# Performance work log

Measured on AMD Instinct MI355X. Metric: run time of the kernel, lower is better.

Reference implementation:

```python
import jax, jax.numpy as jnp
import numpy as np

MUL = 512
IR_DIMS = (1, 3, 5)          # 0e, 1e, 2e -> 2l+1
PW = MUL ** -0.5             # path_weight = (mul_in * n_paths_to_out)^-0.5, n_paths=1 each


def setup_inputs() -> dict:
    key = jax.random.key(0)
    k_x, k0, k1, k2 = jax.random.split(key, 4)
    B = 4096
    D = MUL * sum(IR_DIMS)  # 4608
    return {
        "x": jax.random.normal(k_x, (B, D), dtype=jnp.float32),
        "w0": jax.random.normal(k0, (MUL, MUL), dtype=jnp.float32),
        "w1": jax.random.normal(k1, (MUL, MUL), dtype=jnp.float32),
        "w2": jax.random.normal(k2, (MUL, MUL), dtype=jnp.float32),
        "b0": jnp.zeros((MUL,), dtype=jnp.float32),  # bias only on scalar 0e irrep
    }


def reference(x, w0, w1, w2, b0):
    B = x.shape[0]
    # split x into per-irrep blocks (B, mul, 2l+1), as Irreps.as_list does
    offs = np.cumsum([0] + [MUL * d for d in IR_DIMS])
    blocks = [x[:, offs[i]:offs[i + 1]].reshape(B, MUL, IR_DIMS[i]) for i in range(3)]
    outs = []
    for blk, w, d in zip(blocks, (w0, w1, w2), IR_DIMS):
        # path_weight * einsum('uw,bui->bwi'), then flatten to mul_ir_out.dim
        o = PW * jnp.einsum('uw,bui->bwi', w, blk)
        outs.append(o.reshape(B, MUL * d))
    # bias instruction: path_weight 1.0, only on the scalar (0e) output irrep
    outs[0] = outs[0] + b0[None, :]
    return jnp.concatenate(outs, axis=-1)
```

## Files before the change

### kernel.cpp

```cpp
#include <hip/hip_runtime.h>


#define BATCH 4096
#define DTOT 4608
#define NMUL 512

typedef __attribute__((ext_vector_type(8))) short short8;
typedef __attribute__((ext_vector_type(8))) unsigned short ushort8;
typedef __attribute__((ext_vector_type(4))) float float4v;

#define XPL_BYTES (9ull * BATCH * NMUL * 2)

__device__ __forceinline__ unsigned short f2bf(float f) {
    unsigned int u = __builtin_bit_cast(unsigned int, f);
    return (unsigned short)((u + 0x7fffu + ((u >> 16) & 1u)) >> 16);
}
__device__ __forceinline__ void gld16(const unsigned short* g, unsigned short* l) {
    __builtin_amdgcn_global_load_lds(
        (const __attribute__((address_space(1))) unsigned int*)(const void*)g,
        (__attribute__((address_space(3))) unsigned int*)(void*)l, 16, 0, 0);
}
__device__ __forceinline__ void waitvm0() {
    asm volatile("s_waitcnt vmcnt(0)" ::: "memory");
}
__device__ __forceinline__ void waitlgkm0() {
    asm volatile("s_waitcnt lgkmcnt(0)" ::: "memory");
}
__device__ __forceinline__ void colmap(int col, int& c, int& u) {
    if (col < 512)       { c = 0; u = col; }
    else if (col < 2048) { int t = col - 512;  c = 1 + t % 3; u = t / 3; }
    else                 { int t = col - 2048; c = 4 + t % 5; u = t / 5; }
}

__global__ __launch_bounds__(256) void prep(const float* __restrict__ x,
                                            const float* __restrict__ w0,
                                            const float* __restrict__ w1,
                                            const float* __restrict__ w2,
                                            unsigned short* __restrict__ Xp,
                                            unsigned short* __restrict__ Wt) {
    __shared__ unsigned short buf[4608];
    const int tid = threadIdx.x;
    const int b = blockIdx.x;
    if (b < BATCH) {
        const int row = b;
        const float4v* src = (const float4v*)(x + (size_t)row * DTOT);
        for (int p = tid; p < DTOT / 4; p += 256) {
            float4v v = src[p];
#pragma unroll
            for (int j = 0; j < 4; ++j) {
                int c, u; colmap(p * 4 + j, c, u);
                buf[c * NMUL + u] = f2bf(v[j]);
            }
        }
        __syncthreads();
        for (int q = tid; q < DTOT / 8; q += 256) {
            const int c = q >> 6, u8 = q & 63;
            *(ushort8*)(Xp + ((size_t)(c * BATCH + row) * NMUL) + u8 * 8) =
                *(const ushort8*)&buf[c * NMUL + u8 * 8];
        }
    } else {
        const int t = b - BATCH;
        const int ch = t >> 6, tt = t & 63;
        const int tk = (tt >> 3) * 64, tn = (tt & 7) * 64;
        const float* W = (ch == 0) ? w0 : (ch == 1) ? w1 : w2;
        const int r0 = tid >> 4, c4 = (tid & 15) * 4;
#pragma unroll
        for (int rr = 0; rr < 4; ++rr) {
            const int row = r0 + rr * 16;
            float4v v = *(const float4v*)(W + (size_t)(tk + row) * NMUL + tn + c4);
#pragma unroll
            for (int j = 0; j < 4; ++j) buf[(c4 + j) * 72 + row] = f2bf(v[j]);
        }
        __syncthreads();
        for (int q = tid; q < 512; q += 256) {
            const int nn = q >> 3, k8 = q & 7;
            *(ushort8*)(Wt + ((size_t)(ch * NMUL + tn + nn) * NMUL) + tk + k8 * 8) =
                *(const ushort8*)&buf[nn * 72 + k8 * 8];
        }
    }
}

template <int MI>
__device__ __forceinline__ void kloop(const unsigned short* __restrict__ Ag,
                                      const unsigned short* __restrict__ Bg,
                                      unsigned short* Aw, unsigned short* Bw,
                                      int lr, int lq, int rsw,
                                      float4v (*acc)[4]) {
    for (int kt = 0; kt < 16; ++kt) {
        const int ko = kt * 32;
#pragma unroll
        for (int p = 0; p < MI; ++p)
            gld16(Ag + (size_t)p * 16 * NMUL + ko, Aw + p * 512);
#pragma unroll
        for (int p = 0; p < 4; ++p)
            gld16(Bg + (size_t)p * 16 * NMUL + ko, Bw + p * 512);
        waitvm0();
        short8 af[MI], bf[4];
#pragma unroll
        for (int mi = 0; mi < MI; ++mi)
            af[mi] = *(const short8*)(Aw + (mi * 16 + lr) * 32 + rsw);
#pragma unroll
        for (int ni = 0; ni < 4; ++ni)
            bf[ni] = *(const short8*)(Bw + (ni * 16 + lr) * 32 + rsw);
        __builtin_amdgcn_s_setprio(1);
#pragma unroll
        for (int mi = 0; mi < MI; ++mi)
#pragma unroll
            for (int ni = 0; ni < 4; ++ni)
                acc[mi][ni] = __builtin_amdgcn_mfma_f32_16x16x32_bf16(
                    af[mi], bf[ni], acc[mi][ni], 0, 0, 0);
        __builtin_amdgcn_s_setprio(0);
        waitlgkm0();
    }
}

template <int D, int XOFF>
__device__ __forceinline__ void epi(int tid, int w, int lr, int lq,
                                    int m0, int n0,
                                    float4v (*acc)[4], float* Cs,
                                    float* __restrict__ out) {
    const float PW = 0.044194173824159216f;
    __syncthreads();
#pragma unroll
    for (int mc = 0; mc < 4; ++mc) {
        if (w < D) {
#pragma unroll
            for (int ni = 0; ni < 4; ++ni)
#pragma unroll
                for (int r = 0; r < 4; ++r)
                    Cs[(lq * 4 + r) * (64 * D) + (ni * 16 + lr) * D + w] =
                        acc[mc][ni][r] * PW;
        }
        __syncthreads();
        constexpr int F4 = 16 * 16 * D;
        for (int f = tid; f < F4; f += 320) {
            const int row = f / (16 * D);
            const int c4  = f % (16 * D);
            *(float4v*)(out + (size_t)(m0 + mc * 16 + row) * DTOT + XOFF + n0 * D + c4 * 4) =
                *(const float4v*)(Cs + f * 4);
        }
        __syncthreads();
    }
}

__global__ __launch_bounds__(320) void gemm_all(const unsigned short* __restrict__ Xp,
                                                const unsigned short* __restrict__ Wt,
                                                const float* __restrict__ b0,
                                                float* __restrict__ out) {
    __shared__ __align__(16) unsigned short As[20480];

    const int hw = blockIdx.x;
    const int xcd = hw & 7, j = hw >> 3;
    const int b = ((xcd + ((j >> 3) << 3)) << 3) + (j & 7);

    const int tid = threadIdx.x;
    const int lane = tid & 63;
    const int w = tid >> 6;
    const int lr = lane & 15;
    const int lq = lane >> 4;
    const int ksw = ((lane & 3) ^ ((lane >> 3) & 3)) * 8;
    const int rsw = (lq ^ ((lr >> 1) & 3)) * 8;

    unsigned short* Aw = As + w * 4096;
    unsigned short* Bw = Aw + 2048;

    const bool isD5 = (b < 512);
    const int rel = isD5 ? b : b - 512;
    const int m0 = (rel >> 3) * 64;
    const int n0 = (rel & 7) * 64;

    float4v acc[4][4];
#pragma unroll
    for (int a = 0; a < 4; ++a)
#pragma unroll
        for (int c = 0; c < 4; ++c) acc[a][c] = (float4v)0.f;

    if (isD5) {
        const unsigned short* Ag =
            Xp + ((size_t)(4 + w) * BATCH + m0 + (lane >> 2)) * NMUL + ksw;
        const unsigned short* Bg =
            Wt + ((size_t)2 * NMUL + n0 + (lane >> 2)) * NMUL + ksw;
        kloop<4>(Ag, Bg, Aw, Bw, lr, lq, rsw, acc);
        epi<5, 2048>(tid, w, lr, lq, m0, n0, acc, (float*)As, out);
    } else {
        if (w < 3) {
            const unsigned short* Ag =
                Xp + ((size_t)(1 + w) * BATCH + m0 + (lane >> 2)) * NMUL + ksw;
            const unsigned short* Bg =
                Wt + ((size_t)1 * NMUL + n0 + (lane >> 2)) * NMUL + ksw;
            kloop<4>(Ag, Bg, Aw, Bw, lr, lq, rsw, acc);
        } else {
            const int mb = m0 + (w - 3) * 32;
            const unsigned short* Ag =
                Xp + ((size_t)0 * BATCH + mb + (lane >> 2)) * NMUL + ksw;
            const unsigned short* Bg =
                Wt + ((size_t)0 * NMUL + n0 + (lane >> 2)) * NMUL + ksw;
            kloop<2>(Ag, Bg, Aw, Bw, lr, lq, rsw, acc);
            const float PW = 0.044194173824159216f;
#pragma unroll
            for (int ni = 0; ni < 4; ++ni) {
                const int col = n0 + ni * 16 + lr;
                const float bias = b0[col];
#pragma unroll
                for (int mi = 0; mi < 2; ++mi)
#pragma unroll
                    for (int r = 0; r < 4; ++r)
                        out[(size_t)(mb + mi * 16 + lq * 4 + r) * DTOT + col] =
                            acc[mi][ni][r] * PW + bias;
            }
        }
        epi<3, 512>(tid, w, lr, lq, m0, n0, acc, (float*)As, out);
    }
}

extern "C" void kernel_launch(void* const* d_in, const int* in_sizes, int n_in,
                              void* d_out, int out_size, void* d_ws, size_t ws_size,
                              hipStream_t stream) {
    const float* x  = (const float*)d_in[0];
    const float* w0 = (const float*)d_in[1];
    const float* w1 = (const float*)d_in[2];
    const float* w2 = (const float*)d_in[3];
    const float* b0 = (const float*)d_in[4];
    float* out = (float*)d_out;

    unsigned short* Xp = (unsigned short*)d_ws;
    unsigned short* Wt = (unsigned short*)((char*)d_ws + XPL_BYTES);

    prep<<<dim3(BATCH + 192), dim3(256), 0, stream>>>(x, w0, w1, w2, Xp, Wt);
    gemm_all<<<dim3(1024), dim3(320), 0, stream>>>(Xp, Wt, b0, out);
}
```

Before: 182.3 us.

## Reorganize GEMM into large shared-B tiles with double-buffered LDS pipeline

The packed X layout is changed so each irrep's components sit interleaved per batch row, which turns each irrep block into one tall GEMM with M = B·(2l+1). The GEMM kernel now uses 512-thread blocks with large tiles (BM×256) that share the B tile across eight waves, replacing per-wave private tiles. Loads are staged with K-step 64 and double-buffered, using partial vmcnt waits so the next tile's loads overlap the current tile's MFMAs. The aim is more operand reuse and less per-wave load latency, at the cost of higher LDS use (128KB), fewer blocks (416) and a more complex epilogue that de-interleaves components through LDS.

```diff
diff --git a/kernel.cpp b/kernel.cpp
--- a/kernel.cpp
+++ b/kernel.cpp
@@ -20,8 +20,9 @@
         (const __attribute__((address_space(1))) unsigned int*)(const void*)g,
         (__attribute__((address_space(3))) unsigned int*)(void*)l, 16, 0, 0);
 }
-__device__ __forceinline__ void waitvm0() {
-    asm volatile("s_waitcnt vmcnt(0)" ::: "memory");
+template <int N>
+__device__ __forceinline__ void waitvm() {
+    asm volatile("s_waitcnt vmcnt(%0)" :: "n"(N) : "memory");
 }
 __device__ __forceinline__ void waitlgkm0() {
     asm volatile("s_waitcnt lgkmcnt(0)" ::: "memory");
@@ -55,7 +56,11 @@
         __syncthreads();
         for (int q = tid; q < DTOT / 8; q += 256) {
             const int c = q >> 6, u8 = q & 63;
-            *(ushort8*)(Xp + ((size_t)(c * BATCH + row) * NMUL) + u8 * 8) =
+            size_t rowg;
+            if (c == 0)      rowg = (size_t)row;
+            else if (c < 4)  rowg = 4096 + (size_t)row * 3 + (c - 1);
+            else             rowg = 16384 + (size_t)row * 5 + (c - 4);
+            *(ushort8*)(Xp + rowg * NMUL + u8 * 8) =
                 *(const ushort8*)&buf[c * NMUL + u8 * 8];
         }
     } else {
@@ -80,137 +85,141 @@
     }
 }
 
-template <int MI>
-__device__ __forceinline__ void kloop(const unsigned short* __restrict__ Ag,
-                                      const unsigned short* __restrict__ Bg,
-                                      unsigned short* Aw, unsigned short* Bw,
-                                      int lr, int lq, int rsw,
-                                      float4v (*acc)[4]) {
-    for (int kt = 0; kt < 16; ++kt) {
-        const int ko = kt * 32;
-#pragma unroll
-        for (int p = 0; p < MI; ++p)
-            gld16(Ag + (size_t)p * 16 * NMUL + ko, Aw + p * 512);
-#pragma unroll
-        for (int p = 0; p < 4; ++p)
-            gld16(Bg + (size_t)p * 16 * NMUL + ko, Bw + p * 512);
-        waitvm0();
-        short8 af[MI], bf[4];
-#pragma unroll
-        for (int mi = 0; mi < MI; ++mi)
-            af[mi] = *(const short8*)(Aw + (mi * 16 + lr) * 32 + rsw);
-#pragma unroll
-        for (int ni = 0; ni < 4; ++ni)
-            bf[ni] = *(const short8*)(Bw + (ni * 16 + lr) * 32 + rsw);
-        __builtin_amdgcn_s_setprio(1);
-#pragma unroll
-        for (int mi = 0; mi < MI; ++mi)
-#pragma unroll
-            for (int ni = 0; ni < 4; ++ni)
-                acc[mi][ni] = __builtin_amdgcn_mfma_f32_16x16x32_bf16(
-                    af[mi], bf[ni], acc[mi][ni], 0, 0, 0);
-        __builtin_amdgcn_s_setprio(0);
-        waitlgkm0();
-    }
-}
-
-template <int D, int XOFF>
-__device__ __forceinline__ void epi(int tid, int w, int lr, int lq,
-                                    int m0, int n0,
-                                    float4v (*acc)[4], float* Cs,
-                                    float* __restrict__ out) {
-    const float PW = 0.044194173824159216f;
-    __syncthreads();
-#pragma unroll
-    for (int mc = 0; mc < 4; ++mc) {
-        if (w < D) {
-#pragma unroll
-            for (int ni = 0; ni < 4; ++ni)
-#pragma unroll
-                for (int r = 0; r < 4; ++r)
-                    Cs[(lq * 4 + r) * (64 * D) + (ni * 16 + lr) * D + w] =
-                        acc[mc][ni][r] * PW;
-        }
-        __syncthreads();
-        constexpr int F4 = 16 * 16 * D;
-        for (int f = tid; f < F4; f += 320) {
-            const int row = f / (16 * D);
-            const int c4  = f % (16 * D);
-            *(float4v*)(out + (size_t)(m0 + mc * 16 + row) * DTOT + XOFF + n0 * D + c4 * 4) =
-                *(const float4v*)(Cs + f * 4);
-        }
-        __syncthreads();
-    }
-}
-
-__global__ __launch_bounds__(320) void gemm_all(const unsigned short* __restrict__ Xp,
-                                                const unsigned short* __restrict__ Wt,
-                                                const float* __restrict__ b0,
-                                                float* __restrict__ out) {
-    __shared__ __align__(16) unsigned short As[20480];
-
-    const int hw = blockIdx.x;
-    const int xcd = hw & 7, j = hw >> 3;
-    const int b = ((xcd + ((j >> 3) << 3)) << 3) + (j & 7);
-
+template <int D, int BM, int ROWBASE, int WCH, int XOFF>
+__device__ __forceinline__ void body(int rel,
+                                     const unsigned short* __restrict__ Xp,
+                                     const unsigned short* __restrict__ Wt,
+                                     const float* __restrict__ b0,
+                                     float* __restrict__ out,
+                                     unsigned short* LDS) {
+    constexpr int MF = BM / 32;
+    constexpr int QA = BM / 8;
     const int tid = threadIdx.x;
     const int lane = tid & 63;
     const int w = tid >> 6;
     const int lr = lane & 15;
     const int lq = lane >> 4;
-    const int ksw = ((lane & 3) ^ ((lane >> 3) & 3)) * 8;
-    const int rsw = (lq ^ ((lr >> 1) & 3)) * 8;
-
-    unsigned short* Aw = As + w * 4096;
-    unsigned short* Bw = Aw + 2048;
-
-    const bool isD5 = (b < 512);
-    const int rel = isD5 ? b : b - 512;
-    const int m0 = (rel >> 3) * 64;
-    const int n0 = (rel & 7) * 64;
-
-    float4v acc[4][4];
-#pragma unroll
-    for (int a = 0; a < 4; ++a)
+    const int wm = (w >> 2) * (BM / 2);
+    const int wn = (w & 3) * 64;
+
+    const int n0 = (rel & 1) * 256;
+    const int m0 = (rel >> 1) * BM;
+
+    const int soff = (lane >> 3) * NMUL + (((lane & 7) ^ (lane >> 3)) * 8);
+    const unsigned short* Ga = Xp + (size_t)(ROWBASE + m0) * NMUL;
+    const unsigned short* Gb = Wt + (size_t)(WCH * 512 + n0) * NMUL;
+
+    float4v acc[MF][4];
+#pragma unroll
+    for (int a = 0; a < MF; ++a)
 #pragma unroll
         for (int c = 0; c < 4; ++c) acc[a][c] = (float4v)0.f;
 
-    if (isD5) {
-        const unsigned short* Ag =
-            Xp + ((size_t)(4 + w) * BATCH + m0 + (lane >> 2)) * NMUL + ksw;
-        const unsigned short* Bg =
-            Wt + ((size_t)2 * NMUL + n0 + (lane >> 2)) * NMUL + ksw;
-        kloop<4>(Ag, Bg, Aw, Bw, lr, lq, rsw, acc);
-        epi<5, 2048>(tid, w, lr, lq, m0, n0, acc, (float*)As, out);
-    } else {
-        if (w < 3) {
-            const unsigned short* Ag =
-                Xp + ((size_t)(1 + w) * BATCH + m0 + (lane >> 2)) * NMUL + ksw;
-            const unsigned short* Bg =
-                Wt + ((size_t)1 * NMUL + n0 + (lane >> 2)) * NMUL + ksw;
-            kloop<4>(Ag, Bg, Aw, Bw, lr, lq, rsw, acc);
+    auto stage = [&](int kt, int buf) {
+        const int ko = kt * 64;
+        unsigned short* Ad = LDS + (buf ? (BM * 64) : 0);
+        unsigned short* Bd = LDS + 2 * BM * 64 + (buf ? 16384 : 0);
+        for (int q = w; q < QA; q += 8)
+            gld16(Ga + (size_t)q * 8 * NMUL + soff + ko, Ad + q * 512);
+#pragma unroll
+        for (int qq = 0; qq < 4; ++qq) {
+            const int qb = w * 4 + qq;
+            gld16(Gb + (size_t)qb * 8 * NMUL + soff + ko, Bd + qb * 512);
+        }
+    };
+
+    stage(0, 0);
+    for (int kt = 0; kt < 8; ++kt) {
+        const int buf = kt & 1;
+        if (kt < 7) stage(kt + 1, buf ^ 1);
+        if (kt < 7) {
+            if (D == 5) { if (w < 4) waitvm<7>(); else waitvm<6>(); }
+            else if (D == 3) waitvm<7>();
+            else waitvm<8>();
         } else {
-            const int mb = m0 + (w - 3) * 32;
-            const unsigned short* Ag =
-                Xp + ((size_t)0 * BATCH + mb + (lane >> 2)) * NMUL + ksw;
-            const unsigned short* Bg =
-                Wt + ((size_t)0 * NMUL + n0 + (lane >> 2)) * NMUL + ksw;
-            kloop<2>(Ag, Bg, Aw, Bw, lr, lq, rsw, acc);
-            const float PW = 0.044194173824159216f;
-#pragma unroll
-            for (int ni = 0; ni < 4; ++ni) {
-                const int col = n0 + ni * 16 + lr;
-                const float bias = b0[col];
-#pragma unroll
-                for (int mi = 0; mi < 2; ++mi)
-#pragma unroll
-                    for (int r = 0; r < 4; ++r)
-                        out[(size_t)(mb + mi * 16 + lq * 4 + r) * DTOT + col] =
-                            acc[mi][ni][r] * PW + bias;
-            }
-        }
-        epi<3, 512>(tid, w, lr, lq, m0, n0, acc, (float*)As, out);
+            waitvm<0>();
+        }
+        __builtin_amdgcn_s_barrier();
+        {
+            const unsigned short* Al = LDS + (buf ? (BM * 64) : 0);
+            const unsigned short* Bl = LDS + 2 * BM * 64 + (buf ? 16384 : 0);
+#pragma unroll
+            for (int kk = 0; kk < 2; ++kk) {
+                const int sw = (((kk * 4 + lq) ^ (lr & 7)) * 8);
+                short8 af[MF], bf[4];
+#pragma unroll
+                for (int mi = 0; mi < MF; ++mi)
+                    af[mi] = *(const short8*)(Al + (wm + mi * 16 + lr) * 64 + sw);
+#pragma unroll
+                for (int ni = 0; ni < 4; ++ni)
+                    bf[ni] = *(const short8*)(Bl + (wn + ni * 16 + lr) * 64 + sw);
+                __builtin_amdgcn_s_setprio(1);
+#pragma unroll
+                for (int mi = 0; mi < MF; ++mi)
+#pragma unroll
+                    for (int ni = 0; ni < 4; ++ni)
+                        acc[mi][ni] = __builtin_amdgcn_mfma_f32_16x16x32_bf16(
+                            af[mi], bf[ni], acc[mi][ni], 0, 0, 0);
+                __builtin_amdgcn_s_setprio(0);
+            }
+        }
+        waitlgkm0();
+        __builtin_amdgcn_s_barrier();
     }
+
+    constexpr int NCH = (D == 1) ? 4 : 2;
+    constexpr int CROWS = BM / NCH;
+    constexpr int CB = CROWS / D;
+    float* Cs = (float*)LDS;
+    const float PW = 0.044194173824159216f;
+    const int bstart = m0 / D;
+
+#pragma unroll
+    for (int c = 0; c < NCH; ++c) {
+#pragma unroll
+        for (int mi = 0; mi < MF; ++mi) {
+            const int fr = wm + mi * 16;
+            if (fr >= c * CROWS && fr < (c + 1) * CROWS) {
+#pragma unroll
+                for (int r_ = 0; r_ < 4; ++r_) {
+                    const int lrow = fr + lq * 4 + r_ - c * CROWS;
+                    const int bl = lrow / D, comp = lrow % D;
+#pragma unroll
+                    for (int ni = 0; ni < 4; ++ni)
+                        Cs[(size_t)(bl * 256 + wn + ni * 16 + lr) * D + comp] =
+                            acc[mi][ni][r_] * PW;
+                }
+            }
+        }
+        __syncthreads();
+        const size_t ob = (size_t)(bstart + c * CB) * DTOT + XOFF + (size_t)n0 * D;
+        for (int idx = tid; idx < CB * 64 * D; idx += 512) {
+            const int bl = idx / (64 * D);
+            const int rem = idx - bl * (64 * D);
+            float4v v = *(const float4v*)(Cs + (size_t)bl * 256 * D + rem * 4);
+            if (D == 1) {
+                float4v bias = *(const float4v*)(b0 + n0 + rem * 4);
+                v = v + bias;
+            }
+            *(float4v*)(out + ob + (size_t)bl * DTOT + rem * 4) = v;
+        }
+        __syncthreads();
+    }
+}
+
+__global__ __launch_bounds__(512) void gemm_all(const unsigned short* __restrict__ Xp,
+                                                const unsigned short* __restrict__ Wt,
+                                                const float* __restrict__ b0,
+                                                float* __restrict__ out) {
+    __shared__ __align__(16) unsigned short LDS[65536];
+
+    const int hw = blockIdx.x;
+    const int x = hw & 7, s = hw >> 3;
+    const int b = 16 * (s >> 1) + 2 * x + (s & 1);
+
+    if (b < 256)      body<5, 160, 16384, 2, 2048>(b, Xp, Wt, b0, out, LDS);
+    else if (b < 384) body<3, 192, 4096, 1, 512>(b - 256, Xp, Wt, b0, out, LDS);
+    else              body<1, 256, 0, 0, 0>(b - 384, Xp, Wt, b0, out, LDS);
 }
 
 extern "C" void kernel_launch(void* const* d_in, const int* in_sizes, int n_in,
@@ -227,5 +236,5 @@
     unsigned short* Wt = (unsigned short*)((char*)d_ws + XPL_BYTES);
 
     prep<<<dim3(BATCH + 192), dim3(256), 0, stream>>>(x, w0, w1, w2, Xp, Wt);
-    gemm_all<<<dim3(1024), dim3(320), 0, stream>>>(Xp, Wt, b0, out);
-}
+    gemm_all<<<dim3(416), dim3(512), 0, stream>>>(Xp, Wt, b0, out);
+}
```

After: 173.4 us. 1.05x faster.
